# Optimization experiments

Hardware: AMD Instinct MI355X
Metric: run time of the kernel (lower is better)

## Reference

```python
import jax, jax.numpy as jnp
import numpy as np

K = 3        # neighbors per point (includes self at distance 0, as in knn_points(x, x))
WEIGHT = 1.0


def setup_inputs() -> dict:
    key = jax.random.key(0)
    k0, k1, k2, k3, k4 = jax.random.split(key, 5)
    B, N = 2, 8192
    return {
        "xyz": jax.random.normal(k0, (B, N, 3), dtype=jnp.float32),
        "rotations": jax.random.normal(k1, (B, N, 4), dtype=jnp.float32),
        "scales": jax.random.normal(k2, (B, N, 3), dtype=jnp.float32),
        "colors": jax.random.normal(k3, (B, N, 45), dtype=jnp.float32),
        "opacity": jax.random.normal(k4, (B, N, 1), dtype=jnp.float32),
    }


def _knn(xyz, k):
    # Brute-force self-KNN: squared euclidean distances, k smallest (sorted ascending).
    sq = jnp.sum(xyz * xyz, axis=-1)                       # [N]
    d = sq[:, None] + sq[None, :] - 2.0 * (xyz @ xyz.T)    # [N, N] squared distances
    neg_d, idx = jax.lax.top_k(-d, k)                      # k nearest -> largest of -d
    return -neg_d, idx                                     # dist_sq [N,K], nn_ind [N,K]


def _sample_loss(xyz, rot, sc, col, op):
    dist_sq, nn_ind = _knn(xyz, K)
    # gather [N,K,C] per attribute, unbiased std over the K neighbors (torch default ddof=1)
    std_mean = lambda a: jnp.std(a[nn_ind], axis=1, ddof=1).mean()
    return (std_mean(rot) + std_mean(sc) + std_mean(op) + std_mean(col)
            + dist_sq.mean())


def reference(xyz, rotations, scales, colors, opacity):
    losses = jax.vmap(_sample_loss)(xyz, rotations, scales, colors, opacity)  # [B]
    return jnp.sum(losses) / xyz.shape[0] * WEIGHT
```

## Files before the change

kernel.cpp:

```cpp
#include <hip/hip_runtime.h>
#include <stdint.h>

#define NPTS 8192
#define BLK 512
#define QPB 32
#define BLKS_PER_BATCH (NPTS / QPB)

typedef __attribute__((ext_vector_type(8)))  short short8;
typedef __attribute__((ext_vector_type(16))) float float16;

__device__ __forceinline__ uint32_t umin32(uint32_t a, uint32_t b) { return a < b ? a : b; }
__device__ __forceinline__ uint32_t umax32(uint32_t a, uint32_t b) { return a > b ? a : b; }

__device__ __forceinline__ void ins3(uint32_t key, uint32_t& k0, uint32_t& k1, uint32_t& k2) {
    uint32_t a = umin32(k0, key);
    uint32_t b = umax32(k0, key);
    k0 = a;
    uint32_t c = umin32(k1, b);
    uint32_t d = umax32(k1, b);
    k1 = c;
    k2 = umin32(k2, d);
}

__device__ __forceinline__ uint16_t f2bf(float x) {
    uint32_t u = __float_as_uint(x);
    return (uint16_t)((u + 0x7FFFu + ((u >> 16) & 1u)) >> 16);
}
__device__ __forceinline__ float bf2f(uint16_t s) {
    return __uint_as_float((uint32_t)s << 16);
}

__global__ __launch_bounds__(256) void pack_kernel(
    const float* __restrict__ xyz, uint4* __restrict__ ws,
    float* __restrict__ out, int total)
{
    int t = blockIdx.x * 256 + threadIdx.x;
    if (t == 0) *out = 0.0f;
    if (t >= total) return;
    int b = t >> 13;
    int n = t & (NPTS - 1);
    const float* p = xyz + ((size_t)b * NPTS + n) * 3;
    float cx = p[0], cy = p[1], cz = p[2];
    uint16_t bhx = f2bf(cx), bhy = f2bf(cy), bhz = f2bf(cz);
    uint16_t blx = f2bf(cx - bf2f(bhx));
    uint16_t bly = f2bf(cy - bf2f(bhy));
    uint16_t blz = f2bf(cz - bf2f(bhz));
    float nc = fmaf(cz, cz, fmaf(cy, cy, cx * cx));
    uint16_t nch = f2bf(nc), ncl = f2bf(nc - bf2f(nch));
    const uint32_t ONE = 0x3F80u;
    uint4 a0, a1;
    a0.x = (uint32_t)bhx | ((uint32_t)bhy << 16);
    a0.y = (uint32_t)bhz | ((uint32_t)blx << 16);
    a0.z = (uint32_t)bly | ((uint32_t)blz << 16);
    a0.w = ONE | (ONE << 16);
    a1.x = (uint32_t)bhx | ((uint32_t)bhy << 16);
    a1.y = (uint32_t)bhz | ((uint32_t)nch << 16);
    a1.z = (uint32_t)ncl;
    a1.w = 0u;
    size_t base = (size_t)b * (2 * NPTS);
    ws[base + n]        = a0;
    ws[base + NPTS + n] = a1;
}

__device__ __forceinline__ float point_contrib(
    int j0, int j1, int j2,
    int lane, float xp, float yp, float zp,
    const float* __restrict__ xb,
    const float* __restrict__ rot, const float* __restrict__ sc,
    const float* __restrict__ col, const float* __restrict__ opac,
    size_t abase, float inv_nb)
{
    int c = lane;
    const float* basep = nullptr;
    int stridec = 0, ch = 0;
    float w = 0.0f;
    if (c < 4)       { basep = rot  + abase * 4;  stridec = 4;  ch = c;     w = inv_nb * (1.0f / 4.0f); }
    else if (c < 7)  { basep = sc   + abase * 3;  stridec = 3;  ch = c - 4; w = inv_nb * (1.0f / 3.0f); }
    else if (c == 7) { basep = opac + abase;      stridec = 1;  ch = 0;     w = inv_nb; }
    else if (c < 53) { basep = col  + abase * 45; stridec = 45; ch = c - 8; w = inv_nb * (1.0f / 45.0f); }

    if (basep != nullptr) {
        float v0 = basep[(size_t)j0 * stridec + ch];
        float v1 = basep[(size_t)j1 * stridec + ch];
        float v2 = basep[(size_t)j2 * stridec + ch];
        float mn = (v0 + v1 + v2) * (1.0f / 3.0f);
        float e0 = v0 - mn, e1 = v1 - mn, e2 = v2 - mn;
        return w * sqrtf((e0 * e0 + e1 * e1 + e2 * e2) * 0.5f);
    }
    if (c == 53) {
        float dx = xb[j0 * 3 + 0] - xp, dy = xb[j0 * 3 + 1] - yp, dz = xb[j0 * 3 + 2] - zp;
        float ds = fmaf(dz, dz, fmaf(dy, dy, dx * dx));
        dx = xb[j1 * 3 + 0] - xp; dy = xb[j1 * 3 + 1] - yp; dz = xb[j1 * 3 + 2] - zp;
        ds += fmaf(dz, dz, fmaf(dy, dy, dx * dx));
        dx = xb[j2 * 3 + 0] - xp; dy = xb[j2 * 3 + 1] - yp; dz = xb[j2 * 3 + 2] - zp;
        ds += fmaf(dz, dz, fmaf(dy, dy, dx * dx));
        return ds * (inv_nb * (1.0f / 3.0f));
    }
    return 0.0f;
}

__global__ __launch_bounds__(BLK) void knn_mfma_kernel(
    const float* __restrict__ xyz,
    const float* __restrict__ rot,
    const float* __restrict__ sc,
    const float* __restrict__ colr,
    const float* __restrict__ opac,
    const uint4* __restrict__ pk,
    float* __restrict__ out,
    float inv_nb)
{
    __shared__ uint32_t keybuf[QPB * 256];
    __shared__ int top3j[QPB * 3];
    __shared__ float blockAcc;

    const int tid  = threadIdx.x;
    const int lane = tid & 63;
    const int wv   = tid >> 6;
    const int qcol = lane & 31;
    const int hl   = lane >> 5;
    const int bb   = blockIdx.x / BLKS_PER_BATCH;
    const int qbase = (blockIdx.x % BLKS_PER_BATCH) * QPB;
    const float* xb = xyz + (size_t)bb * NPTS * 3;
    const uint4* pkb = pk + (size_t)bb * (2 * NPTS);

    if (tid == 0) blockAcc = 0.0f;

    const int qm = qbase + qcol;
    const float qx = xb[qm * 3 + 0], qy = xb[qm * 3 + 1], qz = xb[qm * 3 + 2];
    const float ax = -2.0f * qx, ay = -2.0f * qy, az = -2.0f * qz;
    const uint16_t ahx = f2bf(ax), ahy = f2bf(ay), ahz = f2bf(az);
    const uint16_t alx = f2bf(ax - bf2f(ahx));
    const uint16_t aly = f2bf(ay - bf2f(ahy));
    const uint16_t alz = f2bf(az - bf2f(ahz));
    const float nqe = fmaf(qz, qz, fmaf(qy, qy, qx * qx)) + 1e-3f;
    const uint16_t nqh = f2bf(nqe), nql = f2bf(nqe - bf2f(nqh));
    short8 A;
    if (hl == 0) {
        A[0] = (short)ahx; A[1] = (short)ahy; A[2] = (short)ahz;
        A[3] = (short)ahx; A[4] = (short)ahy; A[5] = (short)ahz;
        A[6] = (short)nqh; A[7] = (short)nql;
    } else {
        A[0] = (short)alx; A[1] = (short)aly; A[2] = (short)alz;
        A[3] = (short)0x3F80; A[4] = (short)0x3F80;
        A[5] = 0; A[6] = 0; A[7] = 0;
    }
    const float16 Z = (float16)0.0f;

    uint32_t k0 = ~0u, k1 = ~0u, k2 = ~0u, k3 = ~0u, k4 = ~0u, k5 = ~0u, k6 = ~0u, k7 = ~0u;
    uint32_t k8 = ~0u, k9 = ~0u, k10 = ~0u, k11 = ~0u, k12 = ~0u, k13 = ~0u, k14 = ~0u, k15 = ~0u;

    const int nstart = wv * 1024;
    const short8* lanep = (const short8*)(pkb + (size_t)hl * NPTS + nstart + qcol);
    const uint32_t nb0 = (uint32_t)(nstart + qcol);
#pragma unroll 2
    for (int t = 0; t < 32; ++t) {
        short8 Bf = lanep[t * 32];
        float16 D = __builtin_amdgcn_mfma_f32_32x32x16_bf16(A, Bf, Z, 0, 0, 0);
        const uint32_t jj = nb0 + (uint32_t)(t * 32);
#define KU(i, ki) ki = umin32(ki, (__float_as_uint(D[i]) & 0xFFFFE000u) | jj)
        KU(0, k0);  KU(1, k1);  KU(2, k2);  KU(3, k3);
        KU(4, k4);  KU(5, k5);  KU(6, k6);  KU(7, k7);
        KU(8, k8);  KU(9, k9);  KU(10, k10); KU(11, k11);
        KU(12, k12); KU(13, k13); KU(14, k14); KU(15, k15);
#undef KU
    }

    {
        const int base = hl * 1024 + wv * 32 + qcol;
        keybuf[base +    0] = k0;   keybuf[base +  256] = k1;
        keybuf[base +  512] = k2;   keybuf[base +  768] = k3;
        keybuf[base + 2048] = k4;   keybuf[base + 2304] = k5;
        keybuf[base + 2560] = k6;   keybuf[base + 2816] = k7;
        keybuf[base + 4096] = k8;   keybuf[base + 4352] = k9;
        keybuf[base + 4608] = k10;  keybuf[base + 4864] = k11;
        keybuf[base + 6144] = k12;  keybuf[base + 6400] = k13;
        keybuf[base + 6656] = k14;  keybuf[base + 6912] = k15;
    }
    __syncthreads();

    {
        const int g = lane >> 4, li = lane & 15;
        const int row = wv * 4 + g;
        uint32_t K0 = ~0u, K1 = ~0u, K2 = ~0u;
#pragma unroll
        for (int s = 0; s < 16; ++s) ins3(keybuf[row * 256 + li + s * 16], K0, K1, K2);
#pragma unroll
        for (int mk = 1; mk < 16; mk <<= 1) {
            uint32_t r0 = (uint32_t)__shfl_xor((int)K0, mk);
            uint32_t r1 = (uint32_t)__shfl_xor((int)K1, mk);
            uint32_t r2 = (uint32_t)__shfl_xor((int)K2, mk);
            ins3(r0, K0, K1, K2);
            ins3(r1, K0, K1, K2);
            ins3(r2, K0, K1, K2);
        }
        if (li == 0) {
            top3j[row * 3 + 0] = (int)(K0 & 8191u);
            top3j[row * 3 + 1] = (int)(K1 & 8191u);
            top3j[row * 3 + 2] = (int)(K2 & 8191u);
        }
    }
    __syncthreads();

    float acc = 0.0f;
    const size_t abase = (size_t)bb * NPTS;
    for (int i = 0; i < 4; ++i) {
        const int q = wv * 4 + i;
        const int j0 = top3j[q * 3 + 0];
        const int j1 = top3j[q * 3 + 1];
        const int j2 = top3j[q * 3 + 2];
        const int qi = qbase + q;
        const float xp = xb[qi * 3 + 0], yp = xb[qi * 3 + 1], zp = xb[qi * 3 + 2];
        acc += point_contrib(j0, j1, j2, lane, xp, yp, zp,
                             xb, rot, sc, colr, opac, abase, inv_nb);
    }

#pragma unroll
    for (int off = 32; off > 0; off >>= 1) acc += __shfl_xor(acc, off);
    if (lane == 0) atomicAdd(&blockAcc, acc);
    __syncthreads();
    if (tid == 0) atomicAdd(out, blockAcc);
}

extern "C" void kernel_launch(void* const* d_in, const int* in_sizes, int n_in,
                              void* d_out, int out_size, void* d_ws, size_t ws_size,
                              hipStream_t stream) {
    const float* xyz  = (const float*)d_in[0];
    const float* rot  = (const float*)d_in[1];
    const float* sc   = (const float*)d_in[2];
    const float* colr = (const float*)d_in[3];
    const float* opac = (const float*)d_in[4];
    float* out = (float*)d_out;

    const int B = in_sizes[0] / (NPTS * 3);
    const float inv_nb = 1.0f / ((float)NPTS * (float)B);
    const int total = B * NPTS;

    pack_kernel<<<dim3((total + 255) / 256), dim3(256), 0, stream>>>(
        xyz, (uint4*)d_ws, out, total);
    knn_mfma_kernel<<<dim3(B * BLKS_PER_BATCH), dim3(BLK), 0, stream>>>(
        xyz, rot, sc, colr, opac, (const uint4*)d_ws, out, inv_nb);
}
```

Measured before the change: 85.74 us.

## Split KNN candidate scan across two blocks and merge in a finish kernel

Each query group's 8192-candidate scan is split into two blocks covering 4096 candidates each. This doubles the grid from 512 to 1024 blocks, giving more parallelism and a shorter per-block critical path. Each block writes its partial top-3 keys to workspace. A new finish kernel merges the two halves, gathers the attributes and accumulates the loss. The cost is an extra kernel launch, a global round-trip for the partial results, and twice the per-block setup and in-block reduction work.

```diff
diff --git a/kernel.cpp b/kernel.cpp
--- a/kernel.cpp
+++ b/kernel.cpp
@@ -4,7 +4,7 @@
 #define NPTS 8192
 #define BLK 512
 #define QPB 32
-#define BLKS_PER_BATCH (NPTS / QPB)
+#define GRPS 256
 
 typedef __attribute__((ext_vector_type(8)))  short short8;
 typedef __attribute__((ext_vector_type(16))) float float16;
@@ -62,68 +62,24 @@
     ws[base + NPTS + n] = a1;
 }
 
-__device__ __forceinline__ float point_contrib(
-    int j0, int j1, int j2,
-    int lane, float xp, float yp, float zp,
-    const float* __restrict__ xb,
-    const float* __restrict__ rot, const float* __restrict__ sc,
-    const float* __restrict__ col, const float* __restrict__ opac,
-    size_t abase, float inv_nb)
-{
-    int c = lane;
-    const float* basep = nullptr;
-    int stridec = 0, ch = 0;
-    float w = 0.0f;
-    if (c < 4)       { basep = rot  + abase * 4;  stridec = 4;  ch = c;     w = inv_nb * (1.0f / 4.0f); }
-    else if (c < 7)  { basep = sc   + abase * 3;  stridec = 3;  ch = c - 4; w = inv_nb * (1.0f / 3.0f); }
-    else if (c == 7) { basep = opac + abase;      stridec = 1;  ch = 0;     w = inv_nb; }
-    else if (c < 53) { basep = col  + abase * 45; stridec = 45; ch = c - 8; w = inv_nb * (1.0f / 45.0f); }
-
-    if (basep != nullptr) {
-        float v0 = basep[(size_t)j0 * stridec + ch];
-        float v1 = basep[(size_t)j1 * stridec + ch];
-        float v2 = basep[(size_t)j2 * stridec + ch];
-        float mn = (v0 + v1 + v2) * (1.0f / 3.0f);
-        float e0 = v0 - mn, e1 = v1 - mn, e2 = v2 - mn;
-        return w * sqrtf((e0 * e0 + e1 * e1 + e2 * e2) * 0.5f);
-    }
-    if (c == 53) {
-        float dx = xb[j0 * 3 + 0] - xp, dy = xb[j0 * 3 + 1] - yp, dz = xb[j0 * 3 + 2] - zp;
-        float ds = fmaf(dz, dz, fmaf(dy, dy, dx * dx));
-        dx = xb[j1 * 3 + 0] - xp; dy = xb[j1 * 3 + 1] - yp; dz = xb[j1 * 3 + 2] - zp;
-        ds += fmaf(dz, dz, fmaf(dy, dy, dx * dx));
-        dx = xb[j2 * 3 + 0] - xp; dy = xb[j2 * 3 + 1] - yp; dz = xb[j2 * 3 + 2] - zp;
-        ds += fmaf(dz, dz, fmaf(dy, dy, dx * dx));
-        return ds * (inv_nb * (1.0f / 3.0f));
-    }
-    return 0.0f;
-}
-
 __global__ __launch_bounds__(BLK) void knn_mfma_kernel(
     const float* __restrict__ xyz,
-    const float* __restrict__ rot,
-    const float* __restrict__ sc,
-    const float* __restrict__ colr,
-    const float* __restrict__ opac,
     const uint4* __restrict__ pk,
-    float* __restrict__ out,
-    float inv_nb)
+    uint32_t* __restrict__ halves)
 {
     __shared__ uint32_t keybuf[QPB * 256];
-    __shared__ int top3j[QPB * 3];
-    __shared__ float blockAcc;
-
     const int tid  = threadIdx.x;
     const int lane = tid & 63;
     const int wv   = tid >> 6;
     const int qcol = lane & 31;
     const int hl   = lane >> 5;
-    const int bb   = blockIdx.x / BLKS_PER_BATCH;
-    const int qbase = (blockIdx.x % BLKS_PER_BATCH) * QPB;
+    const int bb   = blockIdx.x / (GRPS * 2);
+    const int rem  = blockIdx.x % (GRPS * 2);
+    const int grp  = rem >> 1;
+    const int half = rem & 1;
+    const int qbase = grp * QPB;
     const float* xb = xyz + (size_t)bb * NPTS * 3;
     const uint4* pkb = pk + (size_t)bb * (2 * NPTS);
-
-    if (tid == 0) blockAcc = 0.0f;
 
     const int qm = qbase + qcol;
     const float qx = xb[qm * 3 + 0], qy = xb[qm * 3 + 1], qz = xb[qm * 3 + 2];
@@ -149,11 +105,11 @@
     uint32_t k0 = ~0u, k1 = ~0u, k2 = ~0u, k3 = ~0u, k4 = ~0u, k5 = ~0u, k6 = ~0u, k7 = ~0u;
     uint32_t k8 = ~0u, k9 = ~0u, k10 = ~0u, k11 = ~0u, k12 = ~0u, k13 = ~0u, k14 = ~0u, k15 = ~0u;
 
-    const int nstart = wv * 1024;
+    const int nstart = half * 4096 + wv * 512;
     const short8* lanep = (const short8*)(pkb + (size_t)hl * NPTS + nstart + qcol);
     const uint32_t nb0 = (uint32_t)(nstart + qcol);
 #pragma unroll 2
-    for (int t = 0; t < 32; ++t) {
+    for (int t = 0; t < 16; ++t) {
         short8 Bf = lanep[t * 32];
         float16 D = __builtin_amdgcn_mfma_f32_32x32x16_bf16(A, Bf, Z, 0, 0, 0);
         const uint32_t jj = nb0 + (uint32_t)(t * 32);
@@ -194,24 +150,81 @@
             ins3(r2, K0, K1, K2);
         }
         if (li == 0) {
-            top3j[row * 3 + 0] = (int)(K0 & 8191u);
-            top3j[row * 3 + 1] = (int)(K1 & 8191u);
-            top3j[row * 3 + 2] = (int)(K2 & 8191u);
+            uint32_t* dst = halves + (size_t)blockIdx.x * (QPB * 3) + row * 3;
+            dst[0] = K0;
+            dst[1] = K1;
+            dst[2] = K2;
         }
     }
+}
+
+__global__ __launch_bounds__(BLK) void finish_kernel(
+    const float* __restrict__ xyz,
+    const float* __restrict__ rot,
+    const float* __restrict__ sc,
+    const float* __restrict__ col,
+    const float* __restrict__ opac,
+    const uint32_t* __restrict__ halves,
+    float* __restrict__ out,
+    float inv_nb)
+{
+    __shared__ float blockAcc;
+    const int tid  = threadIdx.x;
+    const int lane = tid & 63;
+    const int wv   = tid >> 6;
+    const int bb   = blockIdx.x / GRPS;
+    const int grp  = blockIdx.x % GRPS;
+    const int qbase = grp * QPB;
+    const float* xb = xyz + (size_t)bb * NPTS * 3;
+    const size_t abase = (size_t)bb * NPTS;
+
+    if (tid == 0) blockAcc = 0.0f;
     __syncthreads();
 
+    const uint32_t* h0 = halves + (size_t)(blockIdx.x * 2 + 0) * (QPB * 3);
+    const uint32_t* h1 = halves + (size_t)(blockIdx.x * 2 + 1) * (QPB * 3);
+
     float acc = 0.0f;
-    const size_t abase = (size_t)bb * NPTS;
     for (int i = 0; i < 4; ++i) {
         const int q = wv * 4 + i;
-        const int j0 = top3j[q * 3 + 0];
-        const int j1 = top3j[q * 3 + 1];
-        const int j2 = top3j[q * 3 + 2];
+        uint32_t K0 = ~0u, K1 = ~0u, K2 = ~0u;
+        ins3(h0[q * 3 + 0], K0, K1, K2);
+        ins3(h0[q * 3 + 1], K0, K1, K2);
+        ins3(h0[q * 3 + 2], K0, K1, K2);
+        ins3(h1[q * 3 + 0], K0, K1, K2);
+        ins3(h1[q * 3 + 1], K0, K1, K2);
+        ins3(h1[q * 3 + 2], K0, K1, K2);
+        const int j0 = (int)(K0 & 8191u);
+        const int j1 = (int)(K1 & 8191u);
+        const int j2 = (int)(K2 & 8191u);
         const int qi = qbase + q;
         const float xp = xb[qi * 3 + 0], yp = xb[qi * 3 + 1], zp = xb[qi * 3 + 2];
-        acc += point_contrib(j0, j1, j2, lane, xp, yp, zp,
-                             xb, rot, sc, colr, opac, abase, inv_nb);
+
+        int c = lane;
+        const float* basep = nullptr;
+        int stridec = 0, ch = 0;
+        float w = 0.0f;
+        if (c < 4)       { basep = rot  + abase * 4;  stridec = 4;  ch = c;     w = inv_nb * (1.0f / 4.0f); }
+        else if (c < 7)  { basep = sc   + abase * 3;  stridec = 3;  ch = c - 4; w = inv_nb * (1.0f / 3.0f); }
+        else if (c == 7) { basep = opac + abase;      stridec = 1;  ch = 0;     w = inv_nb; }
+        else if (c < 53) { basep = col  + abase * 45; stridec = 45; ch = c - 8; w = inv_nb * (1.0f / 45.0f); }
+
+        if (basep != nullptr) {
+            float v0 = basep[(size_t)j0 * stridec + ch];
+            float v1 = basep[(size_t)j1 * stridec + ch];
+            float v2 = basep[(size_t)j2 * stridec + ch];
+            float mn = (v0 + v1 + v2) * (1.0f / 3.0f);
+            float e0 = v0 - mn, e1 = v1 - mn, e2 = v2 - mn;
+            acc += w * sqrtf((e0 * e0 + e1 * e1 + e2 * e2) * 0.5f);
+        } else if (c == 53) {
+            float dx = xb[j0 * 3 + 0] - xp, dy = xb[j0 * 3 + 1] - yp, dz = xb[j0 * 3 + 2] - zp;
+            float ds = fmaf(dz, dz, fmaf(dy, dy, dx * dx));
+            dx = xb[j1 * 3 + 0] - xp; dy = xb[j1 * 3 + 1] - yp; dz = xb[j1 * 3 + 2] - zp;
+            ds += fmaf(dz, dz, fmaf(dy, dy, dx * dx));
+            dx = xb[j2 * 3 + 0] - xp; dy = xb[j2 * 3 + 1] - yp; dz = xb[j2 * 3 + 2] - zp;
+            ds += fmaf(dz, dz, fmaf(dy, dy, dx * dx));
+            acc += ds * (inv_nb * (1.0f / 3.0f));
+        }
     }
 
 #pragma unroll
@@ -235,8 +248,13 @@
     const float inv_nb = 1.0f / ((float)NPTS * (float)B);
     const int total = B * NPTS;
 
+    uint4* pk = (uint4*)d_ws;
+    uint32_t* halves = (uint32_t*)((char*)d_ws + (1 << 20));
+
     pack_kernel<<<dim3((total + 255) / 256), dim3(256), 0, stream>>>(
-        xyz, (uint4*)d_ws, out, total);
-    knn_mfma_kernel<<<dim3(B * BLKS_PER_BATCH), dim3(BLK), 0, stream>>>(
-        xyz, rot, sc, colr, opac, (const uint4*)d_ws, out, inv_nb);
-}
+        xyz, pk, out, total);
+    knn_mfma_kernel<<<dim3(B * GRPS * 2), dim3(BLK), 0, stream>>>(
+        xyz, (const uint4*)pk, halves);
+    finish_kernel<<<dim3(B * GRPS), dim3(BLK), 0, stream>>>(
+        xyz, rot, sc, colr, opac, (const uint32_t*)halves, out, inv_nb);
+}
```

New measurement: 91.01 us. 6.1% more time.
